# Optimization experiments

Hardware: AMD Instinct MI355X
Metric: run time of the kernel (lower is better)

Reference implementation:

```python
import jax, jax.numpy as jnp
import numpy as np

N = 50000   # nodes
E = 800000  # edges (avg degree 16)
D = 128     # in_feats == out_feats


def setup_inputs() -> dict:
    key = jax.random.key(0)
    k1, k2, k3, k4 = jax.random.split(key, 4)
    h = jax.random.normal(k1, (N, D), dtype=jnp.float32)
    src = jax.random.randint(k2, (E,), 0, N, dtype=jnp.int32)
    dst = jax.random.randint(k3, (E,), 0, N, dtype=jnp.int32)
    snorm_n = jnp.ones((N, 1), dtype=jnp.float32)  # sqrt(1/N) replicated; identity-scaled here
    # NodeApply linear: Linear(2*D, D) with bias
    W = jax.random.normal(k4, (D, 2 * D), dtype=jnp.float32) / np.sqrt(2 * D).astype(np.float32)
    b = jnp.zeros((D,), dtype=jnp.float32)
    return {"h": h, "snorm_n": snorm_n, "W": W, "b": b, "src": src, "dst": dst}


def reference(h, snorm_n, W, b, src, dst):
    # dropout p=0.0 -> identity
    h_in = h
    # gather neighbor messages and segment-mean aggregate (MeanAggregator)
    ones = jnp.ones((src.shape[0],), dtype=h.dtype)
    deg = jax.ops.segment_sum(ones, dst, num_segments=N)            # [N]
    msg_sum = jax.ops.segment_sum(h[src], dst, num_segments=N)     # [N, D]
    c = msg_sum / jnp.maximum(deg, 1.0)[:, None]                   # zero-degree nodes -> c = 0
    # NodeApply: concat -> linear -> L2 normalize -> relu
    bundle = jnp.concatenate([h, c], axis=1) @ W.T + b             # [N, D]
    nrm = jnp.sqrt(jnp.sum(bundle * bundle, axis=1, keepdims=True))
    bundle = bundle / jnp.maximum(nrm, 1e-12)                      # F.normalize(p=2, dim=1)
    out = jax.nn.relu(bundle)
    # graph norm
    out = out * snorm_n
    # residual (in_feats == out_feats)
    return h_in + out
```

## Files before the change

kernel.cpp:

```cpp
#include <hip/hip_runtime.h>
#include <hip/hip_bf16.h>

#define TPB 256
#define CHUNK_LOG 13
#define CHUNK (1 << CHUNK_LOG)
#define HSTRIDE 12544

typedef __attribute__((ext_vector_type(8))) short bf16x8;
typedef __attribute__((ext_vector_type(4))) float f32x4;
typedef __attribute__((ext_vector_type(2))) float f32x2;

__device__ inline unsigned short f2bf(float f) {
    unsigned u = __float_as_uint(f);
    unsigned r = u + 0x7fffu + ((u >> 16) & 1u);
    return (unsigned short)(r >> 16);
}
__device__ inline float bf2f(unsigned short s) {
    return __uint_as_float(((unsigned)s) << 16);
}

__global__ void k_conv(const float* __restrict__ h, const float* __restrict__ W,
                       unsigned short* __restrict__ h_hi, unsigned* __restrict__ h8,
                       unsigned short* __restrict__ Wb, unsigned* ctr, int N) {
    if (blockIdx.x == 0 && threadIdx.x == 0) *ctr = 0u;
    int t = blockIdx.x * TPB + threadIdx.x;
    int nh4 = N * 32;
    if (t < nh4) {
        float4 v = ((const float4*)h)[t];
        ushort4 hi;
        hi.x = f2bf(v.x); hi.y = f2bf(v.y);
        hi.z = f2bf(v.z); hi.w = f2bf(v.w);
        ((ushort4*)h_hi)[t] = hi;
        int p8 = __builtin_amdgcn_cvt_pk_fp8_f32(v.x, v.y, 0, false);
        p8 = __builtin_amdgcn_cvt_pk_fp8_f32(v.z, v.w, p8, true);
        h8[t] = (unsigned)p8;
    } else if (t - nh4 < 8192) {
        int w4 = t - nh4;
        float4 v = ((const float4*)W)[w4];
        ushort4 hi;
        hi.x = f2bf(v.x); hi.y = f2bf(v.y);
        hi.z = f2bf(v.z); hi.w = f2bf(v.w);
        ((ushort4*)Wb)[w4] = hi;
    }
}

__global__ void k_hist(const int* __restrict__ dst,
                       unsigned* __restrict__ hist32, unsigned char* __restrict__ lrank,
                       int E) {
    __shared__ unsigned lhist[HSTRIDE];
    int b = blockIdx.x;
    for (int i = threadIdx.x; i < HSTRIDE; i += TPB) lhist[i] = 0;
    __syncthreads();
    int e0 = b << CHUNK_LOG;
    int e1 = min(e0 + CHUNK, E);
    for (int e = e0 + (int)threadIdx.x; e < e1; e += TPB) {
        int d = dst[e];
        unsigned sh = (d & 3) * 8;
        unsigned old = atomicAdd(&lhist[d >> 2], 1u << sh);
        lrank[e] = (unsigned char)((old >> sh) & 0xffu);
    }
    __syncthreads();
    for (int i = threadIdx.x; i < HSTRIDE; i += TPB)
        hist32[(size_t)b * HSTRIDE + i] = lhist[i];
}

__launch_bounds__(TPB)
__global__ void k_scan(const unsigned* __restrict__ hist32,
                       unsigned short* __restrict__ cbase,
                       int* __restrict__ bsum, unsigned* ctr,
                       int* __restrict__ offs, int N, int E, int NBH) {
    extern __shared__ unsigned tile[];
    __shared__ int sdata[4];
    __shared__ int sb[TPB];
    __shared__ int wsum[4];
    int NB = gridDim.x;
    int bid = blockIdx.x, tid = threadIdx.x;
    int lane = tid & 63, w = tid >> 6;

    int tileBase = bid * 64;
    int total = NBH * 64;
    for (int i = tid; i < total; i += TPB) {
        int b = i >> 6, c = i & 63;
        tile[i] = hist32[(size_t)b * HSTRIDE + tileBase + c];
    }
    __syncthreads();
    int n = bid * TPB + tid;
    unsigned sh = (tid & 3) * 8;
    int wcol = tid >> 2;
    int run = 0;
    for (int b = 0; b < NBH; ++b) {
        int c = (int)((tile[b * 64 + wcol] >> sh) & 0xffu);
        if (n < N) cbase[(size_t)b * N + n] = (unsigned short)run;
        run += c;
    }
    int dv = (n < N) ? run : 0;

    int s = dv;
    for (int o = 32; o; o >>= 1) s += __shfl_xor(s, o);
    if (lane == 0) sdata[w] = s;
    __syncthreads();
    if (tid == 0) {
        int tot = sdata[0] + sdata[1] + sdata[2] + sdata[3];
        __hip_atomic_store(&bsum[bid], tot, __ATOMIC_RELAXED, __HIP_MEMORY_SCOPE_AGENT);
        __hip_atomic_fetch_add(ctr, 1u, __ATOMIC_RELEASE, __HIP_MEMORY_SCOPE_AGENT);
        while (__hip_atomic_load(ctr, __ATOMIC_ACQUIRE, __HIP_MEMORY_SCOPE_AGENT)
               < (unsigned)NB)
            __builtin_amdgcn_s_sleep(2);
    }
    __syncthreads();

    int v = 0;
    if (tid < NB)
        v = __hip_atomic_load(&bsum[tid], __ATOMIC_RELAXED, __HIP_MEMORY_SCOPE_AGENT);
    int x = v;
    for (int o = 1; o < 64; o <<= 1) { int y = __shfl_up(x, o); if (lane >= o) x += y; }
    if (lane == 63) wsum[w] = x;
    __syncthreads();
    int add = 0;
    for (int k = 0; k < w; ++k) add += wsum[k];
    sb[tid] = add + x - v;
    __syncthreads();
    int base = sb[bid];

    int y2 = dv;
    for (int o = 1; o < 64; o <<= 1) { int z = __shfl_up(y2, o); if (lane >= o) y2 += z; }
    __syncthreads();
    if (lane == 63) wsum[w] = y2;
    __syncthreads();
    int add2 = 0;
    for (int k = 0; k < w; ++k) add2 += wsum[k];
    int ex = base + add2 + y2 - dv;
    if (n < N) offs[n] = ex;
    if (n == N - 1) offs[N] = E;
}

__global__ void k_scatter(const int* __restrict__ src, const int* __restrict__ dst,
                          const unsigned char* __restrict__ lrank,
                          const unsigned short* __restrict__ cbase,
                          const int* __restrict__ offs,
                          unsigned short* __restrict__ esrc, int N, int E, int nchunk) {
    int slice = blockIdx.x & 7;
    int chunk = blockIdx.x >> 3;
    int lo = (int)((long long)N * slice >> 3);
    int hi = (int)((long long)N * (slice + 1) >> 3);
    for (int e = chunk * TPB + threadIdx.x; e < E; e += nchunk * TPB) {
        int d = dst[e];
        if (d >= lo && d < hi) {
            int b = e >> CHUNK_LOG;
            int pos = offs[d] + (int)cbase[(size_t)b * N + d] + (int)lrank[e];
            esrc[pos] = (unsigned short)src[e];
        }
    }
}

__global__ void k_agg(const unsigned short* __restrict__ h8s, const int* __restrict__ offs,
                      const unsigned short* __restrict__ esrc,
                      unsigned* __restrict__ c, int N) {
    int wid = (blockIdx.x * TPB + threadIdx.x) >> 6;
    int lane = threadIdx.x & 63;
    if (wid >= N) return;
    int beg = offs[wid], end = offs[wid + 1];
    float ax0 = 0.f, ay0 = 0.f, ax1 = 0.f, ay1 = 0.f;
    int e = beg;
    for (; e + 3 < end; e += 4) {
        int s0 = esrc[e], s1 = esrc[e + 1], s2 = esrc[e + 2], s3 = esrc[e + 3];
        int a0 = h8s[(size_t)s0 * 64 + lane];
        int a1 = h8s[(size_t)s1 * 64 + lane];
        int a2 = h8s[(size_t)s2 * 64 + lane];
        int a3 = h8s[(size_t)s3 * 64 + lane];
        f32x2 f0 = __builtin_amdgcn_cvt_pk_f32_fp8(a0, false);
        f32x2 f1 = __builtin_amdgcn_cvt_pk_f32_fp8(a1, false);
        f32x2 f2 = __builtin_amdgcn_cvt_pk_f32_fp8(a2, false);
        f32x2 f3 = __builtin_amdgcn_cvt_pk_f32_fp8(a3, false);
        ax0 += f0.x + f1.x; ay0 += f0.y + f1.y;
        ax1 += f2.x + f3.x; ay1 += f2.y + f3.y;
    }
    for (; e < end; ++e) {
        int a0 = h8s[(size_t)esrc[e] * 64 + lane];
        f32x2 f0 = __builtin_amdgcn_cvt_pk_f32_fp8(a0, false);
        ax0 += f0.x; ay0 += f0.y;
    }
    float ax = ax0 + ax1, ay = ay0 + ay1;
    float inv = 1.0f / fmaxf((float)(end - beg), 1.0f);
    unsigned pk = ((unsigned)f2bf(ay * inv) << 16) | (unsigned)f2bf(ax * inv);
    c[(size_t)wid * 64 + lane] = pk;
}

__launch_bounds__(TPB)
__global__ void k_apply(const unsigned short* __restrict__ h_hi,
                        const unsigned short* __restrict__ c,
                        const unsigned short* __restrict__ Wb,
                        const float* __restrict__ bia,
                        const float* __restrict__ snorm,
                        float* __restrict__ out, int N) {
    int lane = threadIdx.x & 63;
    int l15 = lane & 15, l4 = lane >> 4;
    int wave = threadIdx.x >> 6;
    int r0 = blockIdx.x * 128 + wave * 32;

    f32x4 acc[2][8] = {};

    #pragma unroll
    for (int kc = 0; kc < 8; ++kc) {
        bf16x8 Bf[8];
        #pragma unroll
        for (int n = 0; n < 8; ++n) {
            Bf[n] = *(const bf16x8*)((const char*)Wb +
                     ((size_t)(n * 16 + l15) * 512 + (size_t)kc * 64 + (size_t)l4 * 16));
        }
        #pragma unroll
        for (int rf = 0; rf < 2; ++rf) {
            int row = r0 + rf * 16 + l15;
            if (row > N - 1) row = N - 1;
            bf16x8 av;
            if (kc < 4) {
                av = *(const bf16x8*)((const char*)h_hi +
                      ((size_t)row * 256 + (size_t)kc * 64 + (size_t)l4 * 16));
            } else {
                av = *(const bf16x8*)((const char*)c +
                      ((size_t)row * 256 + (size_t)(kc - 4) * 64 + (size_t)l4 * 16));
            }
            #pragma unroll
            for (int n = 0; n < 8; ++n)
                acc[rf][n] = __builtin_amdgcn_mfma_f32_16x16x32_bf16(av, Bf[n], acc[rf][n], 0, 0, 0);
        }
    }

    float bn[8];
    #pragma unroll
    for (int n = 0; n < 8; ++n) bn[n] = bia[n * 16 + l15];

    #pragma unroll
    for (int rf = 0; rf < 2; ++rf) {
        float sq[4] = {0.f, 0.f, 0.f, 0.f};
        #pragma unroll
        for (int n = 0; n < 8; ++n) {
            #pragma unroll
            for (int g = 0; g < 4; ++g) {
                acc[rf][n][g] += bn[n];
                sq[g] += acc[rf][n][g] * acc[rf][n][g];
            }
        }
        #pragma unroll
        for (int g = 0; g < 4; ++g) {
            sq[g] += __shfl_xor(sq[g], 1);
            sq[g] += __shfl_xor(sq[g], 2);
            sq[g] += __shfl_xor(sq[g], 4);
            sq[g] += __shfl_xor(sq[g], 8);
        }
        #pragma unroll
        for (int g = 0; g < 4; ++g) {
            int row = r0 + rf * 16 + l4 * 4 + g;
            if (row < N) {
                float invn = 1.0f / fmaxf(sqrtf(sq[g]), 1e-12f);
                float sn = snorm[row];
                #pragma unroll
                for (int n = 0; n < 8; ++n) {
                    int col = n * 16 + l15;
                    float res = bf2f(h_hi[(size_t)row * 128 + col]);
                    out[(size_t)row * 128 + col] =
                        fmaxf(acc[rf][n][g] * invn, 0.f) * sn + res;
                }
            }
        }
    }
}

extern "C" void kernel_launch(void* const* d_in, const int* in_sizes, int n_in,
                              void* d_out, int out_size, void* d_ws, size_t ws_size,
                              hipStream_t stream) {
    const float* h     = (const float*)d_in[0];
    const float* snorm = (const float*)d_in[1];
    const float* W     = (const float*)d_in[2];
    const float* b     = (const float*)d_in[3];
    const int*   src   = (const int*)d_in[4];
    const int*   dst   = (const int*)d_in[5];
    int N = in_sizes[1];
    int E = in_sizes[4];
    float* out = (float*)d_out;

    char* ws = (char*)d_ws;
    size_t off = 0;
    auto alloc = [&](size_t bytes) {
        void* ptr = ws + off;
        off = (off + bytes + 255) & ~(size_t)255;
        return ptr;
    };
    int NB  = (N + TPB - 1) / TPB;
    int NBH = (E + CHUNK - 1) >> CHUNK_LOG;
    int* offs   = (int*)alloc((size_t)(N + 1) * 4);
    int* bsum   = (int*)alloc((size_t)NB * 4);
    unsigned* ctr          = (unsigned*)alloc(256);
    unsigned* hist32       = (unsigned*)alloc((size_t)NBH * HSTRIDE * 4);
    unsigned short* cbase  = (unsigned short*)alloc((size_t)NBH * N * 2);
    unsigned char*  lrank  = (unsigned char*)alloc((size_t)E);
    unsigned short* esrc   = (unsigned short*)alloc((size_t)E * 2);
    unsigned short* h_hi   = (unsigned short*)alloc((size_t)N * 128 * 2);
    unsigned*       h8     = (unsigned*)alloc((size_t)N * 128);
    unsigned short* Wb     = (unsigned short*)alloc((size_t)128 * 256 * 2);
    unsigned* c = hist32;

    int conv_blocks = (N * 32 + 8192 + TPB - 1) / TPB;
    k_conv<<<conv_blocks, TPB, 0, stream>>>(h, W, h_hi, h8, Wb, ctr, N);

    k_hist<<<NBH, TPB, 0, stream>>>(dst, hist32, lrank, E);

    size_t tile_bytes = (size_t)NBH * 64 * 4;
    k_scan<<<NB, TPB, tile_bytes, stream>>>(hist32, cbase, bsum, ctr, offs, N, E, NBH);

    int nchunk = 512;
    k_scatter<<<8 * nchunk, TPB, 0, stream>>>(src, dst, lrank, cbase, offs, esrc, N, E, nchunk);

    k_agg<<<((size_t)N * 64 + TPB - 1) / TPB, TPB, 0, stream>>>((const unsigned short*)h8,
                                                                offs, esrc, c, N);

    int nblk = (N + 127) / 128;
    k_apply<<<nblk, TPB, 0, stream>>>(h_hi, (const unsigned short*)c, Wb, b, snorm, out, N);
}
```

Baseline: 116.5 us.

## Fuse feature conversion into scatter kernel and aggregate two nodes per wave

The standalone conversion kernel (fp32 h and W to bf16/fp8) is folded into the scatter kernel as a grid-stride prologue, and the counter reset becomes a memset. This removes a launch and lets the conversion traffic share a kernel with the scatter. The aggregation kernel now assigns one half-wave per node, with each lane loading 4 fp8 bytes instead of 2, halving the wave count and widening per-lane loads. The risk is that the scatter kernel gets longer, and half-wave nodes with different degrees diverge within a wave.

```diff
diff --git a/kernel.cpp b/kernel.cpp
--- a/kernel.cpp
+++ b/kernel.cpp
@@ -17,31 +17,6 @@
 }
 __device__ inline float bf2f(unsigned short s) {
     return __uint_as_float(((unsigned)s) << 16);
-}
-
-__global__ void k_conv(const float* __restrict__ h, const float* __restrict__ W,
-                       unsigned short* __restrict__ h_hi, unsigned* __restrict__ h8,
-                       unsigned short* __restrict__ Wb, unsigned* ctr, int N) {
-    if (blockIdx.x == 0 && threadIdx.x == 0) *ctr = 0u;
-    int t = blockIdx.x * TPB + threadIdx.x;
-    int nh4 = N * 32;
-    if (t < nh4) {
-        float4 v = ((const float4*)h)[t];
-        ushort4 hi;
-        hi.x = f2bf(v.x); hi.y = f2bf(v.y);
-        hi.z = f2bf(v.z); hi.w = f2bf(v.w);
-        ((ushort4*)h_hi)[t] = hi;
-        int p8 = __builtin_amdgcn_cvt_pk_fp8_f32(v.x, v.y, 0, false);
-        p8 = __builtin_amdgcn_cvt_pk_fp8_f32(v.z, v.w, p8, true);
-        h8[t] = (unsigned)p8;
-    } else if (t - nh4 < 8192) {
-        int w4 = t - nh4;
-        float4 v = ((const float4*)W)[w4];
-        ushort4 hi;
-        hi.x = f2bf(v.x); hi.y = f2bf(v.y);
-        hi.z = f2bf(v.z); hi.w = f2bf(v.w);
-        ((ushort4*)Wb)[w4] = hi;
-    }
 }
 
 __global__ void k_hist(const int* __restrict__ dst,
@@ -134,11 +109,37 @@
     if (n == N - 1) offs[N] = E;
 }
 
-__global__ void k_scatter(const int* __restrict__ src, const int* __restrict__ dst,
-                          const unsigned char* __restrict__ lrank,
-                          const unsigned short* __restrict__ cbase,
-                          const int* __restrict__ offs,
-                          unsigned short* __restrict__ esrc, int N, int E, int nchunk) {
+__global__ void k_scatterconv(const float* __restrict__ h, const float* __restrict__ W,
+                              const int* __restrict__ src, const int* __restrict__ dst,
+                              const unsigned char* __restrict__ lrank,
+                              const unsigned short* __restrict__ cbase,
+                              const int* __restrict__ offs,
+                              unsigned short* __restrict__ esrc,
+                              unsigned short* __restrict__ h_hi,
+                              unsigned* __restrict__ h8,
+                              unsigned short* __restrict__ Wb,
+                              int N, int E, int nchunk) {
+    int nh4 = N * 32;
+    int totalc = nh4 + 8192;
+    for (int t = blockIdx.x * TPB + threadIdx.x; t < totalc; t += gridDim.x * TPB) {
+        if (t < nh4) {
+            float4 v = ((const float4*)h)[t];
+            ushort4 hi;
+            hi.x = f2bf(v.x); hi.y = f2bf(v.y);
+            hi.z = f2bf(v.z); hi.w = f2bf(v.w);
+            ((ushort4*)h_hi)[t] = hi;
+            int p8 = __builtin_amdgcn_cvt_pk_fp8_f32(v.x, v.y, 0, false);
+            p8 = __builtin_amdgcn_cvt_pk_fp8_f32(v.z, v.w, p8, true);
+            h8[t] = (unsigned)p8;
+        } else {
+            int w4 = t - nh4;
+            float4 v = ((const float4*)W)[w4];
+            ushort4 hi;
+            hi.x = f2bf(v.x); hi.y = f2bf(v.y);
+            hi.z = f2bf(v.z); hi.w = f2bf(v.w);
+            ((ushort4*)Wb)[w4] = hi;
+        }
+    }
     int slice = blockIdx.x & 7;
     int chunk = blockIdx.x >> 3;
     int lo = (int)((long long)N * slice >> 3);
@@ -153,37 +154,47 @@
     }
 }
 
-__global__ void k_agg(const unsigned short* __restrict__ h8s, const int* __restrict__ offs,
+__global__ void k_agg(const unsigned* __restrict__ h8, const int* __restrict__ offs,
                       const unsigned short* __restrict__ esrc,
                       unsigned* __restrict__ c, int N) {
-    int wid = (blockIdx.x * TPB + threadIdx.x) >> 6;
-    int lane = threadIdx.x & 63;
-    if (wid >= N) return;
-    int beg = offs[wid], end = offs[wid + 1];
-    float ax0 = 0.f, ay0 = 0.f, ax1 = 0.f, ay1 = 0.f;
+    int wav = (blockIdx.x * TPB + threadIdx.x) >> 6;
+    int half = (threadIdx.x >> 5) & 1;
+    int hl = threadIdx.x & 31;
+    int n = wav * 2 + half;
+    if (n >= N) return;
+    int beg = offs[n], end = offs[n + 1];
+    float a0 = 0.f, a1 = 0.f, a2 = 0.f, a3 = 0.f;
     int e = beg;
     for (; e + 3 < end; e += 4) {
         int s0 = esrc[e], s1 = esrc[e + 1], s2 = esrc[e + 2], s3 = esrc[e + 3];
-        int a0 = h8s[(size_t)s0 * 64 + lane];
-        int a1 = h8s[(size_t)s1 * 64 + lane];
-        int a2 = h8s[(size_t)s2 * 64 + lane];
-        int a3 = h8s[(size_t)s3 * 64 + lane];
-        f32x2 f0 = __builtin_amdgcn_cvt_pk_f32_fp8(a0, false);
-        f32x2 f1 = __builtin_amdgcn_cvt_pk_f32_fp8(a1, false);
-        f32x2 f2 = __builtin_amdgcn_cvt_pk_f32_fp8(a2, false);
-        f32x2 f3 = __builtin_amdgcn_cvt_pk_f32_fp8(a3, false);
-        ax0 += f0.x + f1.x; ay0 += f0.y + f1.y;
-        ax1 += f2.x + f3.x; ay1 += f2.y + f3.y;
+        unsigned u0 = h8[(size_t)s0 * 32 + hl];
+        unsigned u1 = h8[(size_t)s1 * 32 + hl];
+        unsigned u2 = h8[(size_t)s2 * 32 + hl];
+        unsigned u3 = h8[(size_t)s3 * 32 + hl];
+        f32x2 p0 = __builtin_amdgcn_cvt_pk_f32_fp8((int)u0, false);
+        f32x2 q0 = __builtin_amdgcn_cvt_pk_f32_fp8((int)u0, true);
+        f32x2 p1 = __builtin_amdgcn_cvt_pk_f32_fp8((int)u1, false);
+        f32x2 q1 = __builtin_amdgcn_cvt_pk_f32_fp8((int)u1, true);
+        f32x2 p2 = __builtin_amdgcn_cvt_pk_f32_fp8((int)u2, false);
+        f32x2 q2 = __builtin_amdgcn_cvt_pk_f32_fp8((int)u2, true);
+        f32x2 p3 = __builtin_amdgcn_cvt_pk_f32_fp8((int)u3, false);
+        f32x2 q3 = __builtin_amdgcn_cvt_pk_f32_fp8((int)u3, true);
+        a0 += p0.x + p1.x + p2.x + p3.x;
+        a1 += p0.y + p1.y + p2.y + p3.y;
+        a2 += q0.x + q1.x + q2.x + q3.x;
+        a3 += q0.y + q1.y + q2.y + q3.y;
     }
     for (; e < end; ++e) {
-        int a0 = h8s[(size_t)esrc[e] * 64 + lane];
-        f32x2 f0 = __builtin_amdgcn_cvt_pk_f32_fp8(a0, false);
-        ax0 += f0.x; ay0 += f0.y;
-    }
-    float ax = ax0 + ax1, ay = ay0 + ay1;
+        unsigned u0 = h8[(size_t)esrc[e] * 32 + hl];
+        f32x2 p0 = __builtin_amdgcn_cvt_pk_f32_fp8((int)u0, false);
+        f32x2 q0 = __builtin_amdgcn_cvt_pk_f32_fp8((int)u0, true);
+        a0 += p0.x; a1 += p0.y; a2 += q0.x; a3 += q0.y;
+    }
     float inv = 1.0f / fmaxf((float)(end - beg), 1.0f);
-    unsigned pk = ((unsigned)f2bf(ay * inv) << 16) | (unsigned)f2bf(ax * inv);
-    c[(size_t)wid * 64 + lane] = pk;
+    unsigned pk0 = ((unsigned)f2bf(a1 * inv) << 16) | (unsigned)f2bf(a0 * inv);
+    unsigned pk1 = ((unsigned)f2bf(a3 * inv) << 16) | (unsigned)f2bf(a2 * inv);
+    c[(size_t)n * 64 + hl * 2]     = pk0;
+    c[(size_t)n * 64 + hl * 2 + 1] = pk1;
 }
 
 __launch_bounds__(TPB)
@@ -300,8 +311,7 @@
     unsigned short* Wb     = (unsigned short*)alloc((size_t)128 * 256 * 2);
     unsigned* c = hist32;
 
-    int conv_blocks = (N * 32 + 8192 + TPB - 1) / TPB;
-    k_conv<<<conv_blocks, TPB, 0, stream>>>(h, W, h_hi, h8, Wb, ctr, N);
+    hipMemsetAsync(ctr, 0, 4, stream);
 
     k_hist<<<NBH, TPB, 0, stream>>>(dst, hist32, lrank, E);
 
@@ -309,10 +319,11 @@
     k_scan<<<NB, TPB, tile_bytes, stream>>>(hist32, cbase, bsum, ctr, offs, N, E, NBH);
 
     int nchunk = 512;
-    k_scatter<<<8 * nchunk, TPB, 0, stream>>>(src, dst, lrank, cbase, offs, esrc, N, E, nchunk);
-
-    k_agg<<<((size_t)N * 64 + TPB - 1) / TPB, TPB, 0, stream>>>((const unsigned short*)h8,
-                                                                offs, esrc, c, N);
+    k_scatterconv<<<8 * nchunk, TPB, 0, stream>>>(h, W, src, dst, lrank, cbase, offs,
+                                                  esrc, h_hi, h8, Wb, N, E, nchunk);
+
+    int aggblk = (N + 7) / 8;
+    k_agg<<<aggblk, TPB, 0, stream>>>(h8, offs, esrc, c, N);
 
     int nblk = (N + 127) / 128;
     k_apply<<<nblk, TPB, 0, stream>>>(h_hi, (const unsigned short*)c, Wb, b, snorm, out, N);
```

After: 109.9 us. 5.7% less time.
